# Performance work log

Hardware: AMD Instinct MI355X
Metric: run time of the kernel (lower is better)

The kernel has to match this reference:

```python
import jax, jax.numpy as jnp
import numpy as np

V, E, H, L, S, B, FE = 50257, 768, 12, 4, 1024, 2, 4
HD = E // H
EPS = 1e-5


def setup_inputs() -> dict:
    key = jax.random.key(0)
    ks = jax.random.split(key, 16)
    def n(k, shape, scale=0.02):
        return jax.random.normal(k, shape, jnp.float32) * scale
    x = jax.random.randint(ks[0], (B, S), 0, V)
    mask = jnp.tril(jnp.ones((S, S), jnp.int32))[None, None]  # (1,1,S,S) causal
    return {
        "x": x,
        "mask": mask,
        "embed_W": n(ks[1], (V, E)),
        "pos_embed": n(ks[2], (1, S, E)),
        "fc_out_W": n(ks[3], (L, E, E)),
        "fc_out_b": jnp.zeros((L, E), jnp.float32),
        "gate_W": n(ks[4], (L, E, E)),
        "gate_b": jnp.zeros((L, E), jnp.float32),
        "ln1_g": jnp.ones((L, E), jnp.float32),
        "ln1_b": jnp.zeros((L, E), jnp.float32),
        "ln2_g": jnp.ones((L, E), jnp.float32),
        "ln2_b": jnp.zeros((L, E), jnp.float32),
        "ff1_W": n(ks[5], (L, E, FE * E)),
        "ff1_b": jnp.zeros((L, FE * E), jnp.float32),
        "ff2_W": n(ks[6], (L, FE * E, E)),
        "ff2_b": jnp.zeros((L, E), jnp.float32),
        "lnf_g": jnp.ones((E,), jnp.float32),
        "lnf_b": jnp.zeros((E,), jnp.float32),
        "head_W": n(ks[7], (E, V)),
    }


def _layernorm(y, g, b):
    m = jnp.mean(y, -1, keepdims=True)
    v = jnp.mean((y - m) ** 2, -1, keepdims=True)
    return (y - m) * jax.lax.rsqrt(v + EPS) * g + b


def reference(x, mask, embed_W, pos_embed, fc_out_W, fc_out_b, gate_W, gate_b,
              ln1_g, ln1_b, ln2_g, ln2_b, ff1_W, ff1_b, ff2_W, ff2_b,
              lnf_g, lnf_b, head_W):
    h = embed_W[x] + pos_embed[:, :x.shape[1], :]  # (B,S,E)
    scale = 1.0 / np.sqrt(HD)
    for i in range(L):
        # NOTE: source never applies the q/k/v Linear layers; heads are split directly.
        q = h.reshape(B, S, H, HD).transpose(0, 2, 1, 3)  # (B,H,S,HD)
        energy = jnp.einsum('bhqd,bhkd->bhqk', q, q)
        energy = jnp.where(mask == 0, jnp.float32(-1e20), energy)
        attn = jax.nn.softmax(energy * scale, axis=-1)
        o = jnp.einsum('bhqk,bhkd->bhqd', attn, q)
        o = o.transpose(0, 2, 1, 3).reshape(B, S, E)
        o = o @ fc_out_W[i] + fc_out_b[i]
        gate = jax.nn.sigmoid(jnp.mean(h, 1, keepdims=True) @ gate_W[i] + gate_b[i])
        h = _layernorm(gate * o + h, ln1_g[i], ln1_b[i])
        ff = jax.nn.gelu(h @ ff1_W[i] + ff1_b[i], approximate=False) @ ff2_W[i] + ff2_b[i]
        h = _layernorm(ff + h, ln2_g[i], ln2_b[i])
    h = _layernorm(h, lnf_g, lnf_b)
    logits = h @ head_W  # (B,S,V)
    return logits
```

## Files before the change

kernel.cpp:

```cpp
#include <hip/hip_runtime.h>
#include <hip/hip_bf16.h>

#define V 50257
#define E 768
#define NH 12
#define NL 4
#define SS 1024
#define BB 2
#define FEE 4
#define HD 64
#define EPSL 1e-5f
#define NPADH 50432

typedef __hip_bfloat16 bf16;
typedef __attribute__((ext_vector_type(8))) short short8;
typedef __attribute__((ext_vector_type(4))) float f32x4;

#define GLD_SRC(p) (const __attribute__((address_space(1))) void*)(p)
#define GLD_DST(p) (__attribute__((address_space(3))) void*)(p)

__global__ __launch_bounds__(256) void embed_kernel(const int* __restrict__ x, const float* __restrict__ eW,
                                                    const float* __restrict__ pos, float* __restrict__ h,
                                                    bf16* __restrict__ hb){
  size_t i = (size_t)blockIdx.x*256 + threadIdx.x;
  if (i >= (size_t)BB*SS*E) return;
  int e = (int)(i % E);
  size_t bs = i / E;
  int s = (int)(bs % SS);
  int tok = x[bs];
  float v = eW[(size_t)tok*E + e] + pos[(size_t)s*E + e];
  h[i] = v;
  hb[i] = __float2bfloat16(v);
}

__global__ __launch_bounds__(256) void cvt_attn(const bf16* __restrict__ hb, bf16* __restrict__ vT){
  __shared__ short t[64][65];
  int bid = blockIdx.x;
  int st = bid & 15, hh = (bid >> 4) % NH, b = bid / (16*NH);
  int s0 = st*64;
  int c = threadIdx.x & 63, rr = threadIdx.x >> 6;
  #pragma unroll
  for (int i = 0; i < 16; ++i){
    int r = rr*16 + i;
    t[r][c] = __builtin_bit_cast(short, hb[(size_t)(b*SS + s0 + r)*E + hh*HD + c]);
  }
  __syncthreads();
  #pragma unroll
  for (int i = 0; i < 16; ++i){
    int d = rr*16 + i;
    vT[(size_t)((b*NH + hh)*HD + d)*SS + s0 + c] = __builtin_bit_cast(bf16, t[c][d]);
  }
}

__global__ __launch_bounds__(256) void attn_mfma(const bf16* __restrict__ hb, const bf16* __restrict__ vT,
                                                 bf16* __restrict__ Ab){
  __shared__ short Qs[64*64];
  __shared__ short Ks[128*64];
  __shared__ short Vs[64*128];
  __shared__ short Ps[4][16*128];
  int tid = threadIdx.x, wave = tid >> 6, lane = tid & 63;
  int bid = blockIdx.x;
  int qt = 15 - (bid & 15);
  int hh = (bid >> 4) % NH, b = bid / (16*NH);
  int q0 = qt*64;
  int l15 = lane & 15, l4 = lane >> 4;
  int sw7 = l15 & 7;

  #pragma unroll
  for (int rnd = 0; rnd < 2; ++rnd){
    int o = rnd*256 + tid; int row = o >> 3; int cs = (((o & 7) ^ (row & 7))*8);
    __builtin_amdgcn_global_load_lds(GLD_SRC(hb + ((size_t)(b*SS + q0 + row)*E + hh*HD + cs)),
                                     GLD_DST(Qs + o*8), 16, 0, 0);
  }

  float mrun[4], lrun[4];
  #pragma unroll
  for (int j = 0; j < 4; ++j){ mrun[j] = -1e30f; lrun[j] = 0.f; }
  f32x4 acco[4] = {};

  int nkt = (qt >> 1) + 1;
  for (int kt = 0; kt < nkt; ++kt){
    int k0 = kt*128;
    __syncthreads();
    #pragma unroll
    for (int rnd = 0; rnd < 4; ++rnd){
      int o = rnd*256 + tid; int row = o >> 3; int cs = (((o & 7) ^ (row & 7))*8);
      __builtin_amdgcn_global_load_lds(GLD_SRC(hb + ((size_t)(b*SS + k0 + row)*E + hh*HD + cs)),
                                       GLD_DST(Ks + o*8), 16, 0, 0);
    }
    #pragma unroll
    for (int rnd = 0; rnd < 4; ++rnd){
      int o = rnd*256 + tid; int row = o >> 4; int cs = (((o & 15) ^ (row & 15))*8);
      __builtin_amdgcn_global_load_lds(GLD_SRC(vT + ((size_t)((b*NH + hh)*HD + row)*SS + k0 + cs)),
                                       GLD_DST(Vs + o*8), 16, 0, 0);
    }
    __syncthreads();

    f32x4 s[8] = {};
    __builtin_amdgcn_s_setprio(1);
    #pragma unroll
    for (int kk = 0; kk < 2; ++kk){
      int slot = kk*4 + l4;
      short8 af = *(const short8*)&Qs[(wave*16 + l15)*64 + ((slot ^ sw7)*8)];
      #pragma unroll
      for (int n = 0; n < 8; ++n){
        short8 bf8 = *(const short8*)&Ks[(n*16 + l15)*64 + ((slot ^ sw7)*8)];
        s[n] = __builtin_amdgcn_mfma_f32_16x16x32_bf16(af, bf8, s[n], 0, 0, 0);
      }
    }
    __builtin_amdgcn_s_setprio(0);

    bool diag = (kt == nkt - 1);
    #pragma unroll
    for (int j = 0; j < 4; ++j){
      int qg = q0 + wave*16 + l4*4 + j;
      float tmax = -1e30f;
      #pragma unroll
      for (int n = 0; n < 8; ++n){
        float v = s[n][j]*0.125f;
        if (diag && (k0 + n*16 + l15) > qg) v = -1e30f;
        s[n][j] = v; tmax = fmaxf(tmax, v);
      }
      tmax = fmaxf(tmax, __shfl_xor(tmax, 1, 64));
      tmax = fmaxf(tmax, __shfl_xor(tmax, 2, 64));
      tmax = fmaxf(tmax, __shfl_xor(tmax, 4, 64));
      tmax = fmaxf(tmax, __shfl_xor(tmax, 8, 64));
      float mnew = fmaxf(mrun[j], tmax);
      float alpha = __expf(mrun[j] - mnew);
      float rsum = 0.f;
      #pragma unroll
      for (int n = 0; n < 8; ++n){
        float p = __expf(s[n][j] - mnew);
        s[n][j] = p; rsum += p;
      }
      rsum += __shfl_xor(rsum, 1, 64);
      rsum += __shfl_xor(rsum, 2, 64);
      rsum += __shfl_xor(rsum, 4, 64);
      rsum += __shfl_xor(rsum, 8, 64);
      lrun[j] = lrun[j]*alpha + rsum;
      mrun[j] = mnew;
      #pragma unroll
      for (int n = 0; n < 4; ++n) acco[n][j] *= alpha;
      int prow = l4*4 + j;
      #pragma unroll
      for (int n = 0; n < 8; ++n){
        bf16 hv = __float2bfloat16(s[n][j]);
        int slot = (n*2 + (l15 >> 3)) ^ prow;
        Ps[wave][prow*128 + slot*8 + (l15 & 7)] = __builtin_bit_cast(short, hv);
      }
    }
    __syncthreads();

    __builtin_amdgcn_s_setprio(1);
    #pragma unroll
    for (int kk = 0; kk < 4; ++kk){
      int slot = kk*4 + l4;
      short8 pa = *(const short8*)&Ps[wave][l15*128 + ((slot ^ l15)*8)];
      #pragma unroll
      for (int n = 0; n < 4; ++n){
        short8 vb = *(const short8*)&Vs[(n*16 + l15)*128 + ((slot ^ l15)*8)];
        acco[n] = __builtin_amdgcn_mfma_f32_16x16x32_bf16(pa, vb, acco[n], 0, 0, 0);
      }
    }
    __builtin_amdgcn_s_setprio(0);
  }

  #pragma unroll
  for (int j = 0; j < 4; ++j){
    float inv = 1.f / lrun[j];
    int qg = q0 + wave*16 + l4*4 + j;
    #pragma unroll
    for (int n = 0; n < 4; ++n){
      Ab[(size_t)(b*SS + qg)*E + hh*HD + n*16 + l15] = __float2bfloat16(acco[n][j]*inv);
    }
  }
}

__global__ __launch_bounds__(256) void hmean1_kernel(const float* __restrict__ h, float* __restrict__ ph){
  int bid = blockIdx.x;
  int ec = bid % 3, tc = (bid/3) & 15, b = bid / 48;
  int e = ec*256 + threadIdx.x;
  float s = 0.f;
  #pragma unroll 8
  for (int t = tc*64; t < tc*64 + 64; ++t) s += h[((size_t)b*SS + t)*E + e];
  ph[((size_t)b*16 + tc)*E + e] = s;
}

__global__ __launch_bounds__(256) void gate1_kernel(const float* __restrict__ ph, const float* __restrict__ gW,
                                                    float* __restrict__ pg){
  int bid = blockIdx.x;
  int ec = bid % 3, kc = (bid/3) & 3, b = bid / 12;
  int nn = ec*256 + threadIdx.x;
  __shared__ float hms[192];
  if (threadIdx.x < 192){
    int k = kc*192 + threadIdx.x;
    float s = 0.f;
    #pragma unroll
    for (int tc = 0; tc < 16; ++tc) s += ph[((size_t)b*16 + tc)*E + k];
    hms[threadIdx.x] = s * (1.0f/SS);
  }
  __syncthreads();
  float acc = 0.f;
  #pragma unroll 8
  for (int j = 0; j < 192; ++j) acc += hms[j] * gW[(size_t)(kc*192 + j)*E + nn];
  pg[((size_t)b*4 + kc)*E + nn] = acc;
}

__global__ __launch_bounds__(256) void wcvt_kernel(const float* __restrict__ W, bf16* __restrict__ Wt,
                                                   int K, int N, int Npad){
  int l = blockIdx.z;
  W  += (size_t)l*K*N;
  Wt += (size_t)l*Npad*K;
  __shared__ float t[32][33];
  int n0 = blockIdx.x*32, k0 = blockIdx.y*32;
  int tx = threadIdx.x & 31, ty8 = threadIdx.x >> 5;
  #pragma unroll
  for (int i = 0; i < 4; ++i){
    int k = k0 + ty8 + i*8, n = n0 + tx;
    t[ty8 + i*8][tx] = (k < K && n < N) ? W[(size_t)k*N + n] : 0.f;
  }
  __syncthreads();
  #pragma unroll
  for (int i = 0; i < 4; ++i){
    int n = n0 + ty8 + i*8, k = k0 + tx;
    if (n < Npad && k < K) Wt[(size_t)n*K + k] = __float2bfloat16(t[tx][ty8 + i*8]);
  }
}

template<int EPI>
__global__ __launch_bounds__(256, 2) void mfma_gemm(const bf16* __restrict__ A, const bf16* __restrict__ Bt,
                                                    const float* __restrict__ bias, void* __restrict__ Cv,
                                                    int M, int N, int Kslice, int Ktot){
  __shared__ short As[2][128*64];
  __shared__ short Bs[2][128*64];
  int tid = threadIdx.x;
  int wave = tid >> 6, lane = tid & 63;
  int wr = wave >> 1, wc = wave & 1;
  int l15 = lane & 15, l4 = lane >> 4;
  int sw7 = l15 & 7;
  int n0 = blockIdx.x * 128, m0 = blockIdx.y * 128;
  size_t koff = (size_t)blockIdx.z * Kslice;
  f32x4 acc[4][4] = {};
  int srow = tid >> 3;
  int sj = tid & 7;
  const int nks = Kslice >> 6;

  #define STAGE128(bsel, kt) do {                                              \
    int kb = (kt)*64;                                                          \
    _Pragma("unroll")                                                          \
    for (int iss = 0; iss < 4; ++iss){                                         \
      int r = srow + iss*32;                                                   \
      int cs = ((sj ^ (r & 7))*8);                                             \
      __builtin_amdgcn_global_load_lds(GLD_SRC(A + (size_t)(m0 + r)*Ktot + koff + kb + cs),  \
                                       GLD_DST(&As[bsel][r*64 + sj*8]), 16, 0, 0);           \
      __builtin_amdgcn_global_load_lds(GLD_SRC(Bt + (size_t)(n0 + r)*Ktot + koff + kb + cs), \
                                       GLD_DST(&Bs[bsel][r*64 + sj*8]), 16, 0, 0);           \
    }                                                                          \
  } while(0)

  STAGE128(0, 0);
  for (int kt = 0; kt < nks; ++kt){
    int cur = kt & 1;
    if (kt + 1 < nks){
      STAGE128(cur ^ 1, kt + 1);
      asm volatile("s_waitcnt vmcnt(8)" ::: "memory");
    } else {
      asm volatile("s_waitcnt vmcnt(0)" ::: "memory");
    }
    __builtin_amdgcn_s_barrier();
    __builtin_amdgcn_sched_barrier(0);
    __builtin_amdgcn_s_setprio(1);
    #pragma unroll
    for (int kk = 0; kk < 2; ++kk){
      int slot = kk*4 + l4;
      short8 af[4], bfr[4];
      #pragma unroll
      for (int m = 0; m < 4; ++m)
        af[m] = *(const short8*)&As[cur][(wr*64 + m*16 + l15)*64 + ((slot ^ sw7)*8)];
      #pragma unroll
      for (int n = 0; n < 4; ++n)
        bfr[n] = *(const short8*)&Bs[cur][(wc*64 + n*16 + l15)*64 + ((slot ^ sw7)*8)];
      #pragma unroll
      for (int m = 0; m < 4; ++m)
        #pragma unroll
        for (int n = 0; n < 4; ++n)
          acc[m][n] = __builtin_amdgcn_mfma_f32_16x16x32_bf16(af[m], bfr[n], acc[m][n], 0, 0, 0);
    }
    __builtin_amdgcn_s_setprio(0);
    __builtin_amdgcn_s_barrier();
    __builtin_amdgcn_sched_barrier(0);
  }
  #undef STAGE128

  float* Cf = (float*)Cv + (size_t)blockIdx.z * M * N;
  int lrow = l4*4;
  #pragma unroll
  for (int m = 0; m < 4; ++m){
    int row = m0 + wr*64 + m*16 + lrow;
    #pragma unroll
    for (int n = 0; n < 4; ++n){
      int col = n0 + wc*64 + n*16 + l15;
      if (col >= N) continue;
      #pragma unroll
      for (int j = 0; j < 4; ++j){
        float v = acc[m][n][j];
        if (EPI == 3){
          v += bias[col];
          v = 0.5f*v*(1.0f + erff(v*0.70710678f));
          ((bf16*)Cv)[(size_t)(row + j)*N + col] = __float2bfloat16(v);
        } else {
          Cf[(size_t)(row + j)*N + col] = v;
        }
      }
    }
  }
}

__global__ __launch_bounds__(512, 2) void gemm256(const bf16* __restrict__ A, const bf16* __restrict__ Bt,
                                                  float* __restrict__ C, int M, int N, int K, int MT){
  __shared__ short As[2][256*64];
  __shared__ short Bs[2][256*64];
  int tid = threadIdx.x;
  int wave = tid >> 6, lane = tid & 63;
  int wr = wave >> 2, wc = wave & 3;
  int l15 = lane & 15, l4 = lane >> 4;
  int sw7 = l15 & 7;

  int lid = blockIdx.x;
  int cpx = gridDim.x >> 3;
  int wg = (lid & 7)*cpx + (lid >> 3);
  int m0 = (wg % MT)*256, n0 = (wg / MT)*256;

  int srow = tid >> 3;
  int sj = tid & 7;
  const int nks = K >> 6;

  #define STAGE256(bsel, kt) do {                                             \
    int kb = (kt)*64;                                                         \
    _Pragma("unroll")                                                         \
    for (int rnd = 0; rnd < 4; ++rnd){                                        \
      int r = rnd*64 + srow;                                                  \
      int cs = ((sj ^ (r & 7))*8);                                            \
      __builtin_amdgcn_global_load_lds(GLD_SRC(A + (size_t)(m0 + r)*K + kb + cs),   \
                                       GLD_DST(&As[bsel][r*64 + sj*8]), 16, 0, 0);  \
      __builtin_amdgcn_global_load_lds(GLD_SRC(Bt + (size_t)(n0 + r)*K + kb + cs),  \
                                       GLD_DST(&Bs[bsel][r*64 + sj*8]), 16, 0, 0);  \
    }                                                                         \
  } while(0)

  f32x4 acc[8][4] = {};
  STAGE256(0, 0);
  for (int kt = 0; kt < nks; ++kt){
    int cur = kt & 1;
    if (kt + 1 < nks){
      STAGE256(cur ^ 1, kt + 1);
      asm volatile("s_waitcnt vmcnt(8)" ::: "memory");
    } else {
      asm volatile("s_waitcnt vmcnt(0)" ::: "memory");
    }
    __builtin_amdgcn_s_barrier();
    __builtin_amdgcn_sched_barrier(0);
    __builtin_amdgcn_s_setprio(1);
    #pragma unroll
    for (int kk = 0; kk < 2; ++kk){
      int slot = kk*4 + l4;
      short8 af[8], bfr[4];
      #pragma unroll
      for (int m = 0; m < 8; ++m)
        af[m] = *(const short8*)&As[cur][(wr*128 + m*16 + l15)*64 + ((slot ^ sw7)*8)];
      #pragma unroll
      for (int n = 0; n < 4; ++n)
        bfr[n] = *(const short8*)&Bs[cur][(wc*64 + n*16 + l15)*64 + ((slot ^ sw7)*8)];
      #pragma unroll
      for (int m = 0; m < 8; ++m)
        #pragma unroll
        for (int n = 0; n < 4; ++n)
          acc[m][n] = __builtin_amdgcn_mfma_f32_16x16x32_bf16(af[m], bfr[n], acc[m][n], 0, 0, 0);
    }
    __builtin_amdgcn_s_setprio(0);
    __builtin_amdgcn_s_barrier();
    __builtin_amdgcn_sched_barrier(0);
  }
  #undef STAGE256

  int lrow = l4*4;
  #pragma unroll
  for (int m = 0; m < 8; ++m){
    int row = m0 + wr*128 + m*16 + lrow;
    #pragma unroll
    for (int n = 0; n < 4; ++n){
      int col = n0 + wc*64 + n*16 + l15;
      if (col >= N) continue;
      #pragma unroll
      for (int j = 0; j < 4; ++j)
        C[(size_t)(row + j)*N + col] = acc[m][n][j];
    }
  }
}

__global__ __launch_bounds__(256) void ln_kernel(const float* __restrict__ parts, int np,
                                                 const float* __restrict__ bias,
                                                 const float* __restrict__ resid,
                                                 const float* __restrict__ pg, const float* __restrict__ gb,
                                                 const float* __restrict__ g, const float* __restrict__ bta,
                                                 float* __restrict__ out, bf16* __restrict__ outb){
  const size_t PS = (size_t)BB*SS*E;
  int row = blockIdx.x;
  int b = row >> 10;
  int tid = threadIdx.x;
  __shared__ float sred[4];
  float y[3];
  float lsum = 0.f;
  #pragma unroll
  for (int i = 0; i < 3; ++i){
    int e = tid + i*256;
    float v = bias ? bias[e] : 0.f;
    for (int p = 0; p < np; ++p) v += parts[(size_t)p*PS + (size_t)row*E + e];
    if (pg){
      float ga = pg[(size_t)(b*4+0)*E + e] + pg[(size_t)(b*4+1)*E + e]
               + pg[(size_t)(b*4+2)*E + e] + pg[(size_t)(b*4+3)*E + e] + gb[e];
      v *= 1.0f / (1.0f + __expf(-ga));
    }
    if (resid) v += resid[(size_t)row*E + e];
    y[i] = v; lsum += v;
  }
  for (int off = 32; off > 0; off >>= 1) lsum += __shfl_down(lsum, off, 64);
  int wid = tid >> 6, lane = tid & 63;
  if (lane == 0) sred[wid] = lsum;
  __syncthreads();
  float mean = (sred[0]+sred[1]+sred[2]+sred[3]) * (1.0f/E);
  __syncthreads();
  float lvar = 0.f;
  #pragma unroll
  for (int i = 0; i < 3; ++i){ float d = y[i]-mean; lvar += d*d; }
  for (int off = 32; off > 0; off >>= 1) lvar += __shfl_down(lvar, off, 64);
  if (lane == 0) sred[wid] = lvar;
  __syncthreads();
  float rstd = rsqrtf((sred[0]+sred[1]+sred[2]+sred[3]) * (1.0f/E) + EPSL);
  __syncthreads();
  #pragma unroll
  for (int i = 0; i < 3; ++i){
    int e = tid + i*256;
    float r = (y[i]-mean)*rstd*g[e] + bta[e];
    out[(size_t)row*E + e] = r;
    if (outb) outb[(size_t)row*E + e] = __float2bfloat16(r);
  }
}

extern "C" void kernel_launch(void* const* d_in, const int* in_sizes, int n_in,
                              void* d_out, int out_size, void* d_ws, size_t ws_size,
                              hipStream_t stream) {
  const int*   x      = (const int*)  d_in[0];
  const float* embedW = (const float*)d_in[2];
  const float* pos    = (const float*)d_in[3];
  const float* fcW    = (const float*)d_in[4];
  const float* fcB    = (const float*)d_in[5];
  const float* gW     = (const float*)d_in[6];
  const float* gB     = (const float*)d_in[7];
  const float* ln1g   = (const float*)d_in[8];
  const float* ln1b   = (const float*)d_in[9];
  const float* ln2g   = (const float*)d_in[10];
  const float* ln2b   = (const float*)d_in[11];
  const float* f1W    = (const float*)d_in[12];
  const float* f1B    = (const float*)d_in[13];
  const float* f2W    = (const float*)d_in[14];
  const float* f2B    = (const float*)d_in[15];
  const float* lnfg   = (const float*)d_in[16];
  const float* lnfb   = (const float*)d_in[17];
  const float* headW  = (const float*)d_in[18];
  float* out = (float*)d_out;

  const size_t BSE = (size_t)BB*SS*E;
  float* h    = (float*)d_ws;
  float* o    = h   + BSE;
  float* tmp  = o   + BSE;
  float* ph   = tmp + 2*BSE;
  float* pg   = ph  + (size_t)BB*16*E;
  bf16* abA   = (bf16*)(pg + (size_t)BB*4*E);
  bf16* abF   = abA + BSE;
  bf16* WfcT  = abF + BSE*FEE;
  bf16* Wf1T  = WfcT + (size_t)NL*E*E;
  bf16* Wf2T  = Wf1T + (size_t)NL*FEE*E*E;
  bf16* WheadT= Wf2T + (size_t)NL*FEE*E*E;
  bf16* hb    = (bf16*)o;
  bf16* vT    = hb + BSE;

  const int rows = BB*SS;

  embed_kernel<<<(int)((BSE + 255)/256), 256, 0, stream>>>(x, embedW, pos, h, hb);

  { dim3 g(E/32, E/32, NL);        wcvt_kernel<<<g, 256, 0, stream>>>(fcW, WfcT, E, E, E); }
  { dim3 g((FEE*E)/32, E/32, NL);  wcvt_kernel<<<g, 256, 0, stream>>>(f1W, Wf1T, E, FEE*E, FEE*E); }
  { dim3 g(E/32, (FEE*E)/32, NL);  wcvt_kernel<<<g, 256, 0, stream>>>(f2W, Wf2T, FEE*E, E, E); }
  { dim3 g(NPADH/32, E/32, 1);     wcvt_kernel<<<g, 256, 0, stream>>>(headW, WheadT, E, V, NPADH); }

  for (int l = 0; l < NL; ++l){
    size_t oEE = (size_t)l*E*E, oE = (size_t)l*E, oFb = (size_t)l*FEE*E;

    hmean1_kernel<<<BB*16*3, 256, 0, stream>>>(h, ph);
    gate1_kernel<<<BB*4*3, 256, 0, stream>>>(ph, gW + oEE, pg);

    cvt_attn<<<BB*NH*16, 256, 0, stream>>>(hb, vT);
    attn_mfma<<<BB*NH*16, 256, 0, stream>>>(hb, vT, abA);

    { dim3 g(E/128, rows/128, 2);
      mfma_gemm<0><<<g, 256, 0, stream>>>(abA, WfcT + oEE, nullptr, tmp, rows, E, E/2, E); }

    ln_kernel<<<rows, 256, 0, stream>>>(tmp, 2, fcB + oE, h, pg, gB + oE,
                                        ln1g + oE, ln1b + oE, h, abA);

    { dim3 g((FEE*E)/128, rows/128, 1);
      mfma_gemm<3><<<g, 256, 0, stream>>>(abA, Wf1T + (size_t)l*FEE*E*E, f1B + oFb, abF, rows, FEE*E, E, E); }

    { dim3 g(E/128, rows/128, 2);
      mfma_gemm<0><<<g, 256, 0, stream>>>(abF, Wf2T + (size_t)l*FEE*E*E, nullptr, tmp, rows, E, FEE*E/2, FEE*E); }

    ln_kernel<<<rows, 256, 0, stream>>>(tmp, 2, f2B + oE, h, nullptr, nullptr,
                                        ln2g + oE, ln2b + oE, h, hb);
  }

  ln_kernel<<<rows, 256, 0, stream>>>(h, 1, nullptr, nullptr, nullptr, nullptr,
                                      lnfg, lnfb, tmp, abA);
  {
    gemm256<<<(rows/256)*(NPADH/256), 512, 0, stream>>>(abA, WheadT, out, rows, V, E, rows/256);
  }
}
```

Before: 1.022 ms.

## Triple-buffer head GEMM with K=32 stages and LDS-staged vectorized epilogue

Restructures the large 256x256 GEMM, likely the vocab head projection, from double-buffered K=64 stages to triple-buffered K=32 stages. Loads now run two tiles ahead with one barrier per iteration, and the launch-bounds occupancy hint of 2 is dropped. The epilogue stages each wave's accumulators through LDS so results go out as 16-byte vector stores instead of scattered scalar stores. The catch is that the XOR swizzle is removed, so LDS reads may hit bank conflicts, and the smaller stages mean more iterations and barriers.

```diff
diff --git a/kernel.cpp b/kernel.cpp
--- a/kernel.cpp
+++ b/kernel.cpp
@@ -15,6 +15,7 @@
 typedef __hip_bfloat16 bf16;
 typedef __attribute__((ext_vector_type(8))) short short8;
 typedef __attribute__((ext_vector_type(4))) float f32x4;
+typedef __attribute__((ext_vector_type(4), aligned(4))) float f32x4a;
 
 #define GLD_SRC(p) (const __attribute__((address_space(1))) void*)(p)
 #define GLD_DST(p) (__attribute__((address_space(3))) void*)(p)
@@ -316,84 +317,90 @@
   }
 }
 
-__global__ __launch_bounds__(512, 2) void gemm256(const bf16* __restrict__ A, const bf16* __restrict__ Bt,
-                                                  float* __restrict__ C, int M, int N, int K, int MT){
-  __shared__ short As[2][256*64];
-  __shared__ short Bs[2][256*64];
+__global__ __launch_bounds__(512) void gemm256(const bf16* __restrict__ A, const bf16* __restrict__ Bt,
+                                               float* __restrict__ C, int M, int N, int K, int MT){
+  __shared__ short As[3][256*32];
+  __shared__ short Bs[3][256*32];
   int tid = threadIdx.x;
   int wave = tid >> 6, lane = tid & 63;
   int wr = wave >> 2, wc = wave & 3;
   int l15 = lane & 15, l4 = lane >> 4;
-  int sw7 = l15 & 7;
 
   int lid = blockIdx.x;
   int cpx = gridDim.x >> 3;
   int wg = (lid & 7)*cpx + (lid >> 3);
   int m0 = (wg % MT)*256, n0 = (wg / MT)*256;
 
-  int srow = tid >> 3;
-  int sj = tid & 7;
-  const int nks = K >> 6;
-
-  #define STAGE256(bsel, kt) do {                                             \
-    int kb = (kt)*64;                                                         \
-    _Pragma("unroll")                                                         \
-    for (int rnd = 0; rnd < 4; ++rnd){                                        \
-      int r = rnd*64 + srow;                                                  \
-      int cs = ((sj ^ (r & 7))*8);                                            \
-      __builtin_amdgcn_global_load_lds(GLD_SRC(A + (size_t)(m0 + r)*K + kb + cs),   \
-                                       GLD_DST(&As[bsel][r*64 + sj*8]), 16, 0, 0);  \
-      __builtin_amdgcn_global_load_lds(GLD_SRC(Bt + (size_t)(n0 + r)*K + kb + cs),  \
-                                       GLD_DST(&Bs[bsel][r*64 + sj*8]), 16, 0, 0);  \
-    }                                                                         \
+  const int nks = K >> 5;
+
+  #define STG(slot, kt) do {                                                          \
+    int kb = (kt)*32;                                                                 \
+    _Pragma("unroll")                                                                 \
+    for (int i = 0; i < 2; ++i){                                                      \
+      int o = i*512 + tid; int r = o >> 2; int sl = o & 3;                            \
+      __builtin_amdgcn_global_load_lds(GLD_SRC(A + (size_t)(m0 + r)*K + kb + sl*8),   \
+                                       GLD_DST(&As[slot][o*8]), 16, 0, 0);            \
+      __builtin_amdgcn_global_load_lds(GLD_SRC(Bt + (size_t)(n0 + r)*K + kb + sl*8),  \
+                                       GLD_DST(&Bs[slot][o*8]), 16, 0, 0);            \
+    }                                                                                 \
   } while(0)
 
   f32x4 acc[8][4] = {};
-  STAGE256(0, 0);
+  STG(0, 0);
+  STG(1, 1);
+  asm volatile("s_waitcnt vmcnt(4)" ::: "memory");
+  __builtin_amdgcn_s_barrier();
+  __builtin_amdgcn_sched_barrier(0);
+
   for (int kt = 0; kt < nks; ++kt){
-    int cur = kt & 1;
+    int cur = kt % 3;
+    if (kt + 2 < nks) STG((kt + 2) % 3, kt + 2);
+    short8 af[8], bfr[4];
+    #pragma unroll
+    for (int m = 0; m < 8; ++m)
+      af[m] = *(const short8*)&As[cur][(wr*128 + m*16 + l15)*32 + l4*8];
+    #pragma unroll
+    for (int n = 0; n < 4; ++n)
+      bfr[n] = *(const short8*)&Bs[cur][(wc*64 + n*16 + l15)*32 + l4*8];
+    __builtin_amdgcn_s_setprio(1);
+    #pragma unroll
+    for (int m = 0; m < 8; ++m)
+      #pragma unroll
+      for (int n = 0; n < 4; ++n)
+        acc[m][n] = __builtin_amdgcn_mfma_f32_16x16x32_bf16(af[m], bfr[n], acc[m][n], 0, 0, 0);
+    __builtin_amdgcn_s_setprio(0);
     if (kt + 1 < nks){
-      STAGE256(cur ^ 1, kt + 1);
-      asm volatile("s_waitcnt vmcnt(8)" ::: "memory");
-    } else {
-      asm volatile("s_waitcnt vmcnt(0)" ::: "memory");
-    }
-    __builtin_amdgcn_s_barrier();
-    __builtin_amdgcn_sched_barrier(0);
-    __builtin_amdgcn_s_setprio(1);
-    #pragma unroll
-    for (int kk = 0; kk < 2; ++kk){
-      int slot = kk*4 + l4;
-      short8 af[8], bfr[4];
-      #pragma unroll
-      for (int m = 0; m < 8; ++m)
-        af[m] = *(const short8*)&As[cur][(wr*128 + m*16 + l15)*64 + ((slot ^ sw7)*8)];
-      #pragma unroll
-      for (int n = 0; n < 4; ++n)
-        bfr[n] = *(const short8*)&Bs[cur][(wc*64 + n*16 + l15)*64 + ((slot ^ sw7)*8)];
-      #pragma unroll
-      for (int m = 0; m < 8; ++m)
+      if (kt + 2 < nks) asm volatile("s_waitcnt vmcnt(4)" ::: "memory");
+      else              asm volatile("s_waitcnt vmcnt(0)" ::: "memory");
+      __builtin_amdgcn_s_barrier();
+      __builtin_amdgcn_sched_barrier(0);
+    }
+  }
+  #undef STG
+
+  __syncthreads();
+  float* sw = ((float*)&As[0][0]) + wave*1104;
+  int rbase = m0 + wr*128;
+  int c0w = n0 + wc*64;
+  #pragma unroll
+  for (int m = 0; m < 8; ++m){
+    #pragma unroll
+    for (int n = 0; n < 4; ++n)
+      #pragma unroll
+      for (int j = 0; j < 4; ++j)
+        sw[(l4*4 + j)*68 + n*16 + l15] = acc[m][n][j];
+    #pragma unroll
+    for (int jj = 0; jj < 4; ++jj){
+      int rl = jj*4 + l4;
+      f32x4a v = *(const f32x4a*)&sw[rl*68 + l15*4];
+      int row = rbase + m*16 + rl;
+      int col = c0w + l15*4;
+      if (col + 3 < N){
+        *(f32x4a*)&C[(size_t)row*N + col] = v;
+      } else {
         #pragma unroll
-        for (int n = 0; n < 4; ++n)
-          acc[m][n] = __builtin_amdgcn_mfma_f32_16x16x32_bf16(af[m], bfr[n], acc[m][n], 0, 0, 0);
-    }
-    __builtin_amdgcn_s_setprio(0);
-    __builtin_amdgcn_s_barrier();
-    __builtin_amdgcn_sched_barrier(0);
-  }
-  #undef STAGE256
-
-  int lrow = l4*4;
-  #pragma unroll
-  for (int m = 0; m < 8; ++m){
-    int row = m0 + wr*128 + m*16 + lrow;
-    #pragma unroll
-    for (int n = 0; n < 4; ++n){
-      int col = n0 + wc*64 + n*16 + l15;
-      if (col >= N) continue;
-      #pragma unroll
-      for (int j = 0; j < 4; ++j)
-        C[(size_t)(row + j)*N + col] = acc[m][n][j];
+        for (int c = 0; c < 4; ++c) if (col + c < N) C[(size_t)row*N + col + c] = v[c];
+      }
     }
   }
 }
```

After: 1.052 ms. +2.9%, slower.
